# Optimization experiments

Measured on AMD Instinct MI355X. Metric: run time of the kernel, lower is better.

## Reference

```python
import jax, jax.numpy as jnp
import numpy as np

N = 50000   # nodes
E = 800000  # edges
D = 128     # feature / hidden dim
G = 64      # graphs in batch
L = 3       # GCN layers
EPS = 1e-5  # LayerNorm eps (torch default)


def setup_inputs() -> dict:
    key = jax.random.key(0)
    ks = jax.random.split(key, 6)
    x = jax.random.normal(ks[0], (N, D), dtype=jnp.float32)
    edge_index = jax.random.randint(ks[1], (2, E), 0, N)
    batch = jnp.sort(jax.random.randint(ks[2], (N,), 0, G))
    Ws = jax.random.normal(ks[3], (L, D, D), dtype=jnp.float32) / np.sqrt(D).astype(np.float32)
    bs = jnp.zeros((L, D), dtype=jnp.float32)
    gammas = jnp.ones((L, D), dtype=jnp.float32)
    betas = jnp.zeros((L, D), dtype=jnp.float32)
    return {"x": x, "edge_index": edge_index, "batch": batch,
            "Ws": Ws, "bs": bs, "gammas": gammas, "betas": betas,
            "num_graphs": G}


def _layernorm(h, g, b):
    mu = jnp.mean(h, axis=-1, keepdims=True)
    var = jnp.mean((h - mu) ** 2, axis=-1, keepdims=True)
    return g * (h - mu) * jax.lax.rsqrt(var + EPS) + b


def reference(x, edge_index, batch, Ws, bs, gammas, betas, num_graphs):
    n = x.shape[0]
    loop = jnp.arange(n)
    # GCNConv adds self-loops; symmetric normalization on augmented graph
    src = jnp.concatenate([edge_index[0], loop])
    dst = jnp.concatenate([edge_index[1], loop])
    deg = jax.ops.segment_sum(jnp.ones_like(dst, dtype=x.dtype), dst, num_segments=n)
    dinv = jax.lax.rsqrt(jnp.maximum(deg, 1.0))  # deg >= 1 via self-loops
    norm_e = dinv[src] * dinv[dst]               # [E+N]

    h = x
    for i in range(Ws.shape[0]):
        hw = h @ Ws[i]                           # [N, D] dense GEMM
        msg = hw[src] * norm_e[:, None]          # gather + edge scale
        h = jax.ops.segment_sum(msg, dst, num_segments=n) + bs[i]  # scatter-add
        h = jax.nn.relu(_layernorm(h, gammas[i], betas[i]))
        # dropout is identity in eval mode

    # global mean pool over graph ids
    s = jax.ops.segment_sum(h, batch, num_segments=num_graphs)
    cnt = jax.ops.segment_sum(jnp.ones((n,), x.dtype), batch, num_segments=num_graphs)
    return s / jnp.maximum(cnt, 1.0)[:, None]
```

## Files before the change

kernel.cpp:

```cpp
#include <hip/hip_runtime.h>
#include <math.h>


#define NDIM 128
#define LN_EPS 1e-5f
#define NGRAPH 64
#define EPB 2048
#define CSR_CAP 8192

typedef __attribute__((ext_vector_type(8))) short short8;
typedef __attribute__((ext_vector_type(8))) ushort ushort8;
typedef __attribute__((ext_vector_type(4))) float f32x4;

__device__ __forceinline__ ushort f2bf(float f) {
    unsigned u = __float_as_uint(f);
    return (ushort)((u + 0x7FFF + ((u >> 16) & 1)) >> 16);
}
__device__ __forceinline__ float bf2f(ushort b) {
    return __uint_as_float(((unsigned)b) << 16);
}

__device__ __forceinline__ uint block_excl_scan(uint v, uint* s) {
    int t = threadIdx.x;
    s[t] = v; __syncthreads();
    #pragma unroll
    for (int off = 1; off < 256; off <<= 1) {
        uint x = (t >= off) ? s[t - off] : 0u;
        __syncthreads();
        s[t] += x;
        __syncthreads();
    }
    uint incl = s[t];
    __syncthreads();
    return incl - v;
}


__global__ __launch_bounds__(256) void k_build1(const int* __restrict__ src, const int* __restrict__ dst,
                                                uint* __restrict__ hist, uint* __restrict__ arena, int E) {
    __shared__ uint h[256], s[256], rank[256];
    int t = threadIdx.x, b = blockIdx.x;
    h[t] = 0; __syncthreads();
    int e0 = b * EPB;
    #pragma unroll
    for (int i = 0; i < 8; i++) {
        int e = e0 + i * 256 + t;
        if (e < E) atomicAdd(&h[((uint)dst[e]) >> 8], 1u);
    }
    __syncthreads();
    uint cnt = h[t];
    uint off = block_excl_scan(cnt, s);
    hist[(size_t)b * 257 + t] = off;
    if (t == 0) hist[(size_t)b * 257 + 256] = (uint)(min(E - e0, EPB));
    rank[t] = off;
    __syncthreads();
    #pragma unroll
    for (int i = 0; i < 8; i++) {
        int e = e0 + i * 256 + t;
        if (e < E) {
            uint d = (uint)dst[e], sv = (uint)src[e];
            uint bin = d >> 8;
            uint r = atomicAdd(&rank[bin], 1u);
            arena[(size_t)b * EPB + r] = (d << 16) | sv;
        }
    }
}


__global__ __launch_bounds__(256) void k_sort2b(const uint* __restrict__ arena, const uint* __restrict__ hist,
                                                const int* __restrict__ batch,
                                                ushort* __restrict__ csr, int2* __restrict__ bd,
                                                float* __restrict__ dinv,
                                                int* __restrict__ gstart, int* __restrict__ gend,
                                                const float* __restrict__ Ws, ushort* __restrict__ Wt,
                                                int N, int NB, int EB) {
    __shared__ uint h[256], nbase[256], s[256];
    __shared__ uint coff[512], csz[512];
    int t = threadIdx.x, b = blockIdx.x;
    if (b >= NB) {
        int l = b - NB;
        const float* wsrc = Ws + (size_t)l * NDIM * NDIM;
        char* o = (char*)(Wt + (size_t)l * NDIM * NDIM);
        for (int idx = t; idx < NDIM * NDIM; idx += 256) {
            int k = idx >> 7, nn = idx & 127;
            int byte = ((nn * NDIM + k) * 2) ^ ((nn & 7) << 4);
            *(ushort*)(o + byte) = f2bf(wsrc[idx]);
        }
        return;
    }
    for (int r = t; r < EB; r += 256) {
        uint o  = hist[(size_t)r * 257 + b];
        uint nx = (b < 255) ? hist[(size_t)r * 257 + b + 1] : hist[(size_t)r * 257 + 256];
        coff[r] = r * EPB + o;
        csz[r]  = nx - o;
    }
    h[t] = 0; __syncthreads();
    for (int r = t; r < EB; r += 256) {
        uint c0 = coff[r], cn = csz[r];
        for (uint j = 0; j < cn; j++)
            atomicAdd(&h[(arena[c0 + j] >> 16) & 255u], 1u);
    }
    __syncthreads();
    uint dg = h[t];
    uint excl = block_excl_scan((dg + 3u) & ~3u, s);
    uint myb = (uint)b * CSR_CAP + excl;
    nbase[t] = myb;
    int n = b * 256 + t;
    if (n < N) {
        bd[n] = make_int2((int)myb, (int)dg);
        dinv[n] = rsqrtf((float)(dg + 1u));
        int g = batch[n];
        if (n == 0 || batch[n - 1] != g) gstart[g] = n;
        if (n == N - 1 || batch[n + 1] != g) gend[g] = n + 1;
    }
    h[t] = 0; __syncthreads();
    for (int r = t; r < EB; r += 256) {
        uint c0 = coff[r], cn = csz[r];
        for (uint j = 0; j < cn; j++) {
            uint e = arena[c0 + j];
            uint bin = (e >> 16) & 255u;
            uint rk = atomicAdd(&h[bin], 1u);
            csr[nbase[bin] + rk] = (ushort)(e & 0xFFFFu);
        }
    }
}


template <bool AF32>
__global__ __launch_bounds__(256) void k_gemm(const void* __restrict__ Ap, const ushort* __restrict__ Wt,
                                              ushort* __restrict__ C, const float* __restrict__ dinv, int N) {
    __shared__ char sW[32768];
    __shared__ ushort sC[64 * NDIM];
    int tid = threadIdx.x;
    {
        const float4* g = (const float4*)Wt;
        float4* s = (float4*)sW;
        #pragma unroll
        for (int i = 0; i < 8; i++) s[tid + 256 * i] = g[tid + 256 * i];
    }
    __syncthreads();

    int wave = tid >> 6, lane = tid & 63;
    int l15 = lane & 15, lhi = lane >> 4;
    int rw = blockIdx.x * 64 + wave * 16;

    f32x4 acc[8];
    #pragma unroll
    for (int n = 0; n < 8; n++) acc[n] = f32x4{0.f, 0.f, 0.f, 0.f};

    const float*  Af = (const float*)Ap;
    const ushort* Ab = (const ushort*)Ap;

    #pragma unroll
    for (int ks = 0; ks < 4; ks++) {
        int k = ks * 32 + lhi * 8;
        short8 a = short8{};
        int r = rw + l15;
        if (r < N) {
            if (AF32) {
                float4 v0 = *(const float4*)&Af[(size_t)r * NDIM + k];
                float4 v1 = *(const float4*)&Af[(size_t)r * NDIM + k + 4];
                short8 t;
                t[0] = (short)f2bf(v0.x); t[1] = (short)f2bf(v0.y);
                t[2] = (short)f2bf(v0.z); t[3] = (short)f2bf(v0.w);
                t[4] = (short)f2bf(v1.x); t[5] = (short)f2bf(v1.y);
                t[6] = (short)f2bf(v1.z); t[7] = (short)f2bf(v1.w);
                a = t;
            } else {
                a = *(const short8*)&Ab[(size_t)r * NDIM + k];
            }
        }
        #pragma unroll
        for (int n = 0; n < 8; n++) {
            int nn = n * 16 + l15;
            int byte = (nn * 256 + k * 2) ^ ((nn & 7) << 4);
            short8 b = *(const short8*)(sW + byte);
            acc[n] = __builtin_amdgcn_mfma_f32_16x16x32_bf16(a, b, acc[n], 0, 0, 0);
        }
    }

    #pragma unroll
    for (int r = 0; r < 4; r++) {
        int row = rw + lhi * 4 + r;
        float dn = (row < N) ? dinv[row] : 0.f;
        #pragma unroll
        for (int n = 0; n < 8; n++)
            sC[(wave * 16 + lhi * 4 + r) * NDIM + n * 16 + l15] = f2bf(acc[n][r] * dn);
    }
    __syncthreads();
    int row0 = blockIdx.x * 64;
    #pragma unroll
    for (int i = 0; i < 4; i++) {
        int flat = tid + i * 256;
        int row = flat >> 4, c8 = (flat & 15) * 8;
        int gr = row0 + row;
        if (gr < N)
            *(short8*)&C[(size_t)gr * NDIM + c8] = *(const short8*)&sC[row * NDIM + c8];
    }
}


__global__ __launch_bounds__(256) void k_agg(const ushort* __restrict__ hw, ushort* __restrict__ out,
                                             const float* __restrict__ dinv, const int2* __restrict__ bd,
                                             const ushort* __restrict__ csr,
                                             const float* __restrict__ bias, const float* __restrict__ gamma,
                                             const float* __restrict__ beta, int N) {
    int gtid = blockIdx.x * 256 + threadIdx.x;
    int n = gtid >> 5;
    int l4 = threadIdx.x & 31;
    if (n >= N) return;

    const ushort4* hv = (const ushort4*)hw;
    ushort4 sv = hv[(size_t)n * 32 + l4];
    float a0 = bf2f(sv.x), a1 = bf2f(sv.y), a2 = bf2f(sv.z), a3 = bf2f(sv.w);

    int2 bdv = bd[n];
    int b0 = bdv.x, dg = bdv.y;
    int nfull = dg & ~7;
    ushort4 sa, sb;
    if (nfull > 0) {
        sa = *(const ushort4*)&csr[b0];
        sb = *(const ushort4*)&csr[b0 + 4];
    }
    for (int i = 0; i < nfull; i += 8) {
        ushort4 ca = sa, cb = sb;
        if (i + 8 < nfull) {
            sa = *(const ushort4*)&csr[b0 + i + 8];
            sb = *(const ushort4*)&csr[b0 + i + 12];
        }
        ushort4 t0 = hv[(size_t)ca.x * 32 + l4];
        ushort4 t1 = hv[(size_t)ca.y * 32 + l4];
        ushort4 t2 = hv[(size_t)ca.z * 32 + l4];
        ushort4 t3 = hv[(size_t)ca.w * 32 + l4];
        ushort4 t4 = hv[(size_t)cb.x * 32 + l4];
        ushort4 t5 = hv[(size_t)cb.y * 32 + l4];
        ushort4 t6 = hv[(size_t)cb.z * 32 + l4];
        ushort4 t7 = hv[(size_t)cb.w * 32 + l4];
        a0 += bf2f(t0.x) + bf2f(t1.x) + bf2f(t2.x) + bf2f(t3.x)
            + bf2f(t4.x) + bf2f(t5.x) + bf2f(t6.x) + bf2f(t7.x);
        a1 += bf2f(t0.y) + bf2f(t1.y) + bf2f(t2.y) + bf2f(t3.y)
            + bf2f(t4.y) + bf2f(t5.y) + bf2f(t6.y) + bf2f(t7.y);
        a2 += bf2f(t0.z) + bf2f(t1.z) + bf2f(t2.z) + bf2f(t3.z)
            + bf2f(t4.z) + bf2f(t5.z) + bf2f(t6.z) + bf2f(t7.z);
        a3 += bf2f(t0.w) + bf2f(t1.w) + bf2f(t2.w) + bf2f(t3.w)
            + bf2f(t4.w) + bf2f(t5.w) + bf2f(t6.w) + bf2f(t7.w);
    }
    for (int i = nfull; i < dg; i++) {
        int s = csr[b0 + i];
        ushort4 t = hv[(size_t)s * 32 + l4];
        a0 += bf2f(t.x); a1 += bf2f(t.y); a2 += bf2f(t.z); a3 += bf2f(t.w);
    }

    float dn = dinv[n];
    a0 *= dn; a1 *= dn; a2 *= dn; a3 *= dn;

    float4 bv = ((const float4*)bias)[l4];
    a0 += bv.x; a1 += bv.y; a2 += bv.z; a3 += bv.w;

    float s1 = a0 + a1 + a2 + a3;
    float s2 = a0 * a0 + a1 * a1 + a2 * a2 + a3 * a3;
    #pragma unroll
    for (int o = 1; o < 32; o <<= 1) {
        s1 += __shfl_xor(s1, o);
        s2 += __shfl_xor(s2, o);
    }
    float mu = s1 * (1.f / NDIM);
    float var = s2 * (1.f / NDIM) - mu * mu;
    float rs = rsqrtf(var + LN_EPS);

    float4 gv = ((const float4*)gamma)[l4];
    float4 be = ((const float4*)beta)[l4];
    ushort4 y;
    y.x = f2bf(fmaxf(gv.x * (a0 - mu) * rs + be.x, 0.f));
    y.y = f2bf(fmaxf(gv.y * (a1 - mu) * rs + be.y, 0.f));
    y.z = f2bf(fmaxf(gv.z * (a2 - mu) * rs + be.z, 0.f));
    y.w = f2bf(fmaxf(gv.w * (a3 - mu) * rs + be.w, 0.f));
    ((ushort4*)out)[(size_t)n * 32 + l4] = y;
}


__global__ __launch_bounds__(256) void k_pool2(const ushort* __restrict__ h, const int* __restrict__ gstart,
                                               const int* __restrict__ gend, float* __restrict__ out) {
    __shared__ float ps[16][128];
    int t = threadIdx.x, g = blockIdx.x;
    int st = gstart[g], en = gend[g];
    int rslot = t >> 4, dc = (t & 15) * 8;
    float acc[8] = {0.f, 0.f, 0.f, 0.f, 0.f, 0.f, 0.f, 0.f};
    for (int r = st + rslot; r < en; r += 16) {
        ushort8 v = *(const ushort8*)&h[(size_t)r * NDIM + dc];
        #pragma unroll
        for (int j = 0; j < 8; j++) acc[j] += bf2f(v[j]);
    }
    #pragma unroll
    for (int j = 0; j < 8; j++) ps[rslot][dc + j] = acc[j];
    __syncthreads();
    if (t < 128) {
        float s = 0.f;
        #pragma unroll
        for (int k = 0; k < 16; k++) s += ps[k][t];
        float c = (float)(en - st);
        out[g * NDIM + t] = s / fmaxf(c, 1.f);
    }
}


extern "C" void kernel_launch(void* const* d_in, const int* in_sizes, int n_in,
                              void* d_out, int out_size, void* d_ws, size_t ws_size,
                              hipStream_t stream) {
    const float* x      = (const float*)d_in[0];
    const int*   ei     = (const int*)d_in[1];
    const int*   batch  = (const int*)d_in[2];
    const float* Ws     = (const float*)d_in[3];
    const float* bs     = (const float*)d_in[4];
    const float* gammas = (const float*)d_in[5];
    const float* betas  = (const float*)d_in[6];
    float* out = (float*)d_out;

    int N = in_sizes[0] / NDIM;
    int E = in_sizes[1] / 2;
    const int* src = ei;
    const int* dst = ei + E;
    int EB = (E + EPB - 1) / EPB;
    int NB = (N + 255) / 256;

    char* w = (char*)d_ws;
    auto alloc = [&](size_t bytes) { char* p = w; w += (bytes + 255) & ~(size_t)255; return p; };
    uint*   hist   = (uint*)alloc((size_t)EB * 257 * 4);
    uint*   arena  = (uint*)alloc((size_t)EB * EPB * 4);
    ushort* csr    = (ushort*)alloc((size_t)NB * CSR_CAP * 2);
    int2*   bd     = (int2*)alloc((size_t)N * 8);
    float*  dinv   = (float*)alloc((size_t)N * 4);
    int*    gse    = (int*)alloc(2 * NGRAPH * 4);
    int*    gstart = gse;
    int*    gend   = gse + NGRAPH;
    ushort* Wt     = (ushort*)alloc((size_t)3 * NDIM * NDIM * 2);
    ushort* bufA   = (ushort*)alloc((size_t)N * NDIM * 2);
    ushort* bufB   = (ushort*)alloc((size_t)N * NDIM * 2);

    k_build1<<<EB, 256, 0, stream>>>(src, dst, hist, arena, E);
    k_sort2b<<<NB + 3, 256, 0, stream>>>(arena, hist, batch, csr, bd, dinv,
                                         gstart, gend, Ws, Wt, N, NB, EB);

    int gGemm = (N + 63) / 64;
    int gAgg  = (N * 32 + 255) / 256;
    for (int l = 0; l < 3; l++) {
        const ushort* wl = Wt + (size_t)l * NDIM * NDIM;
        if (l == 0)
            k_gemm<true><<<gGemm, 256, 0, stream>>>((const void*)x, wl, bufB, dinv, N);
        else
            k_gemm<false><<<gGemm, 256, 0, stream>>>((const void*)bufA, wl, bufB, dinv, N);
        k_agg<<<gAgg, 256, 0, stream>>>(bufB, bufA, dinv, bd, csr,
                                        bs + l * NDIM, gammas + l * NDIM, betas + l * NDIM, N);
    }

    k_pool2<<<NGRAPH, 256, 0, stream>>>(bufA, gstart, gend, out);
}
```

Before: 272.4 us.

## Fuse aggregation+LayerNorm of layer i with GEMM of layer i+1

```diff
diff --git a/kernel.cpp b/kernel.cpp
--- a/kernel.cpp
+++ b/kernel.cpp
@@ -126,9 +126,8 @@
 }
 
 
-template <bool AF32>
-__global__ __launch_bounds__(256) void k_gemm(const void* __restrict__ Ap, const ushort* __restrict__ Wt,
-                                              ushort* __restrict__ C, const float* __restrict__ dinv, int N) {
+__global__ __launch_bounds__(256) void k_gemm0(const float* __restrict__ Af, const ushort* __restrict__ Wt,
+                                               ushort* __restrict__ C, const float* __restrict__ dinv, int N) {
     __shared__ char sW[32768];
     __shared__ ushort sC[64 * NDIM];
     int tid = threadIdx.x;
@@ -148,27 +147,20 @@
     #pragma unroll
     for (int n = 0; n < 8; n++) acc[n] = f32x4{0.f, 0.f, 0.f, 0.f};
 
-    const float*  Af = (const float*)Ap;
-    const ushort* Ab = (const ushort*)Ap;
-
     #pragma unroll
     for (int ks = 0; ks < 4; ks++) {
         int k = ks * 32 + lhi * 8;
         short8 a = short8{};
         int r = rw + l15;
         if (r < N) {
-            if (AF32) {
-                float4 v0 = *(const float4*)&Af[(size_t)r * NDIM + k];
-                float4 v1 = *(const float4*)&Af[(size_t)r * NDIM + k + 4];
-                short8 t;
-                t[0] = (short)f2bf(v0.x); t[1] = (short)f2bf(v0.y);
-                t[2] = (short)f2bf(v0.z); t[3] = (short)f2bf(v0.w);
-                t[4] = (short)f2bf(v1.x); t[5] = (short)f2bf(v1.y);
-                t[6] = (short)f2bf(v1.z); t[7] = (short)f2bf(v1.w);
-                a = t;
-            } else {
-                a = *(const short8*)&Ab[(size_t)r * NDIM + k];
-            }
+            float4 v0 = *(const float4*)&Af[(size_t)r * NDIM + k];
+            float4 v1 = *(const float4*)&Af[(size_t)r * NDIM + k + 4];
+            short8 t;
+            t[0] = (short)f2bf(v0.x); t[1] = (short)f2bf(v0.y);
+            t[2] = (short)f2bf(v0.z); t[3] = (short)f2bf(v0.w);
+            t[4] = (short)f2bf(v1.x); t[5] = (short)f2bf(v1.y);
+            t[6] = (short)f2bf(v1.z); t[7] = (short)f2bf(v1.w);
+            a = t;
         }
         #pragma unroll
         for (int n = 0; n < 8; n++) {
@@ -200,82 +192,138 @@
 }
 
 
-__global__ __launch_bounds__(256) void k_agg(const ushort* __restrict__ hw, ushort* __restrict__ out,
-                                             const float* __restrict__ dinv, const int2* __restrict__ bd,
-                                             const ushort* __restrict__ csr,
-                                             const float* __restrict__ bias, const float* __restrict__ gamma,
-                                             const float* __restrict__ beta, int N) {
-    int gtid = blockIdx.x * 256 + threadIdx.x;
-    int n = gtid >> 5;
-    int l4 = threadIdx.x & 31;
-    if (n >= N) return;
-
-    const ushort4* hv = (const ushort4*)hw;
-    ushort4 sv = hv[(size_t)n * 32 + l4];
-    float a0 = bf2f(sv.x), a1 = bf2f(sv.y), a2 = bf2f(sv.z), a3 = bf2f(sv.w);
-
-    int2 bdv = bd[n];
-    int b0 = bdv.x, dg = bdv.y;
-    int nfull = dg & ~7;
-    ushort4 sa, sb;
-    if (nfull > 0) {
-        sa = *(const ushort4*)&csr[b0];
-        sb = *(const ushort4*)&csr[b0 + 4];
-    }
-    for (int i = 0; i < nfull; i += 8) {
-        ushort4 ca = sa, cb = sb;
-        if (i + 8 < nfull) {
-            sa = *(const ushort4*)&csr[b0 + i + 8];
-            sb = *(const ushort4*)&csr[b0 + i + 12];
-        }
-        ushort4 t0 = hv[(size_t)ca.x * 32 + l4];
-        ushort4 t1 = hv[(size_t)ca.y * 32 + l4];
-        ushort4 t2 = hv[(size_t)ca.z * 32 + l4];
-        ushort4 t3 = hv[(size_t)ca.w * 32 + l4];
-        ushort4 t4 = hv[(size_t)cb.x * 32 + l4];
-        ushort4 t5 = hv[(size_t)cb.y * 32 + l4];
-        ushort4 t6 = hv[(size_t)cb.z * 32 + l4];
-        ushort4 t7 = hv[(size_t)cb.w * 32 + l4];
-        a0 += bf2f(t0.x) + bf2f(t1.x) + bf2f(t2.x) + bf2f(t3.x)
-            + bf2f(t4.x) + bf2f(t5.x) + bf2f(t6.x) + bf2f(t7.x);
-        a1 += bf2f(t0.y) + bf2f(t1.y) + bf2f(t2.y) + bf2f(t3.y)
-            + bf2f(t4.y) + bf2f(t5.y) + bf2f(t6.y) + bf2f(t7.y);
-        a2 += bf2f(t0.z) + bf2f(t1.z) + bf2f(t2.z) + bf2f(t3.z)
-            + bf2f(t4.z) + bf2f(t5.z) + bf2f(t6.z) + bf2f(t7.z);
-        a3 += bf2f(t0.w) + bf2f(t1.w) + bf2f(t2.w) + bf2f(t3.w)
-            + bf2f(t4.w) + bf2f(t5.w) + bf2f(t6.w) + bf2f(t7.w);
-    }
-    for (int i = nfull; i < dg; i++) {
-        int s = csr[b0 + i];
-        ushort4 t = hv[(size_t)s * 32 + l4];
-        a0 += bf2f(t.x); a1 += bf2f(t.y); a2 += bf2f(t.z); a3 += bf2f(t.w);
-    }
-
-    float dn = dinv[n];
-    a0 *= dn; a1 *= dn; a2 *= dn; a3 *= dn;
-
-    float4 bv = ((const float4*)bias)[l4];
-    a0 += bv.x; a1 += bv.y; a2 += bv.z; a3 += bv.w;
-
-    float s1 = a0 + a1 + a2 + a3;
-    float s2 = a0 * a0 + a1 * a1 + a2 * a2 + a3 * a3;
-    #pragma unroll
-    for (int o = 1; o < 32; o <<= 1) {
-        s1 += __shfl_xor(s1, o);
-        s2 += __shfl_xor(s2, o);
-    }
-    float mu = s1 * (1.f / NDIM);
-    float var = s2 * (1.f / NDIM) - mu * mu;
-    float rs = rsqrtf(var + LN_EPS);
-
-    float4 gv = ((const float4*)gamma)[l4];
-    float4 be = ((const float4*)beta)[l4];
-    ushort4 y;
-    y.x = f2bf(fmaxf(gv.x * (a0 - mu) * rs + be.x, 0.f));
-    y.y = f2bf(fmaxf(gv.y * (a1 - mu) * rs + be.y, 0.f));
-    y.z = f2bf(fmaxf(gv.z * (a2 - mu) * rs + be.z, 0.f));
-    y.w = f2bf(fmaxf(gv.w * (a3 - mu) * rs + be.w, 0.f));
-    ((ushort4*)out)[(size_t)n * 32 + l4] = y;
+template <bool GEMM>
+__global__ __launch_bounds__(256) void k_fused(const ushort* __restrict__ hw_in, ushort* __restrict__ outbuf,
+                                               const float* __restrict__ dinv, const int2* __restrict__ bd,
+                                               const ushort* __restrict__ csr,
+                                               const float* __restrict__ bias, const float* __restrict__ gamma,
+                                               const float* __restrict__ beta,
+                                               const ushort* __restrict__ Wt, int N) {
+    __shared__ char sW[32768];
+    __shared__ ushort sA[64 * NDIM];
+    int tid = threadIdx.x;
+    if (GEMM) {
+        const float4* g = (const float4*)Wt;
+        float4* s = (float4*)sW;
+        #pragma unroll
+        for (int i = 0; i < 8; i++) s[tid + 256 * i] = g[tid + 256 * i];
+    }
+
+    int nb = blockIdx.x * 64;
+    int hwid = tid >> 5, l4 = tid & 31;
+    const ushort4* hv = (const ushort4*)hw_in;
+    const float4 bv = ((const float4*)bias)[l4];
+    const float4 gv = ((const float4*)gamma)[l4];
+    const float4 be = ((const float4*)beta)[l4];
+
+    for (int i = 0; i < 8; i++) {
+        int n = nb + hwid * 8 + i;
+        ushort4 y = make_ushort4(0, 0, 0, 0);
+        if (n < N) {
+            ushort4 sv = hv[(size_t)n * 32 + l4];
+            float a0 = bf2f(sv.x), a1 = bf2f(sv.y), a2 = bf2f(sv.z), a3 = bf2f(sv.w);
+            int2 bdv = bd[n];
+            int b0 = bdv.x, dg = bdv.y;
+            int nfull = dg & ~7;
+            ushort4 sa, sb;
+            if (nfull > 0) {
+                sa = *(const ushort4*)&csr[b0];
+                sb = *(const ushort4*)&csr[b0 + 4];
+            }
+            for (int j = 0; j < nfull; j += 8) {
+                ushort4 ca = sa, cb = sb;
+                if (j + 8 < nfull) {
+                    sa = *(const ushort4*)&csr[b0 + j + 8];
+                    sb = *(const ushort4*)&csr[b0 + j + 12];
+                }
+                ushort4 t0 = hv[(size_t)ca.x * 32 + l4];
+                ushort4 t1 = hv[(size_t)ca.y * 32 + l4];
+                ushort4 t2 = hv[(size_t)ca.z * 32 + l4];
+                ushort4 t3 = hv[(size_t)ca.w * 32 + l4];
+                ushort4 t4 = hv[(size_t)cb.x * 32 + l4];
+                ushort4 t5 = hv[(size_t)cb.y * 32 + l4];
+                ushort4 t6 = hv[(size_t)cb.z * 32 + l4];
+                ushort4 t7 = hv[(size_t)cb.w * 32 + l4];
+                a0 += bf2f(t0.x) + bf2f(t1.x) + bf2f(t2.x) + bf2f(t3.x)
+                    + bf2f(t4.x) + bf2f(t5.x) + bf2f(t6.x) + bf2f(t7.x);
+                a1 += bf2f(t0.y) + bf2f(t1.y) + bf2f(t2.y) + bf2f(t3.y)
+                    + bf2f(t4.y) + bf2f(t5.y) + bf2f(t6.y) + bf2f(t7.y);
+                a2 += bf2f(t0.z) + bf2f(t1.z) + bf2f(t2.z) + bf2f(t3.z)
+                    + bf2f(t4.z) + bf2f(t5.z) + bf2f(t6.z) + bf2f(t7.z);
+                a3 += bf2f(t0.w) + bf2f(t1.w) + bf2f(t2.w) + bf2f(t3.w)
+                    + bf2f(t4.w) + bf2f(t5.w) + bf2f(t6.w) + bf2f(t7.w);
+            }
+            for (int j = nfull; j < dg; j++) {
+                int s = csr[b0 + j];
+                ushort4 t = hv[(size_t)s * 32 + l4];
+                a0 += bf2f(t.x); a1 += bf2f(t.y); a2 += bf2f(t.z); a3 += bf2f(t.w);
+            }
+            float dn = dinv[n];
+            a0 = a0 * dn + bv.x; a1 = a1 * dn + bv.y;
+            a2 = a2 * dn + bv.z; a3 = a3 * dn + bv.w;
+            float s1 = a0 + a1 + a2 + a3;
+            float s2 = a0 * a0 + a1 * a1 + a2 * a2 + a3 * a3;
+            #pragma unroll
+            for (int o = 1; o < 32; o <<= 1) {
+                s1 += __shfl_xor(s1, o);
+                s2 += __shfl_xor(s2, o);
+            }
+            float mu = s1 * (1.f / NDIM);
+            float var = s2 * (1.f / NDIM) - mu * mu;
+            float rs = rsqrtf(var + LN_EPS);
+            y.x = f2bf(fmaxf(gv.x * (a0 - mu) * rs + be.x, 0.f));
+            y.y = f2bf(fmaxf(gv.y * (a1 - mu) * rs + be.y, 0.f));
+            y.z = f2bf(fmaxf(gv.z * (a2 - mu) * rs + be.z, 0.f));
+            y.w = f2bf(fmaxf(gv.w * (a3 - mu) * rs + be.w, 0.f));
+        }
+        if (GEMM) {
+            int row = hwid * 8 + i;
+            int byte = (row * 256 + 8 * l4) ^ ((row & 7) << 4);
+            *(ushort4*)((char*)sA + byte) = y;
+        } else if (n < N) {
+            ((ushort4*)outbuf)[(size_t)n * 32 + l4] = y;
+        }
+    }
+    if (!GEMM) return;
+    __syncthreads();
+
+    int wave = tid >> 6, lane = tid & 63;
+    int l15 = lane & 15, lhi = lane >> 4;
+    f32x4 acc[8];
+    #pragma unroll
+    for (int n = 0; n < 8; n++) acc[n] = f32x4{0.f, 0.f, 0.f, 0.f};
+    #pragma unroll
+    for (int ks = 0; ks < 4; ks++) {
+        int k = ks * 32 + lhi * 8;
+        int rloc = wave * 16 + l15;
+        short8 a = *(const short8*)((char*)sA + ((rloc * 256 + k * 2) ^ ((rloc & 7) << 4)));
+        #pragma unroll
+        for (int n = 0; n < 8; n++) {
+            int nn = n * 16 + l15;
+            int byte = (nn * 256 + k * 2) ^ ((nn & 7) << 4);
+            short8 b = *(const short8*)(sW + byte);
+            acc[n] = __builtin_amdgcn_mfma_f32_16x16x32_bf16(a, b, acc[n], 0, 0, 0);
+        }
+    }
+    __syncthreads();
+    #pragma unroll
+    for (int r = 0; r < 4; r++) {
+        int rloc = wave * 16 + lhi * 4 + r;
+        int row = nb + rloc;
+        float dn = (row < N) ? dinv[row] : 0.f;
+        #pragma unroll
+        for (int n = 0; n < 8; n++)
+            sA[rloc * NDIM + n * 16 + l15] = f2bf(acc[n][r] * dn);
+    }
+    __syncthreads();
+    #pragma unroll
+    for (int i = 0; i < 4; i++) {
+        int flat = tid + i * 256;
+        int row = flat >> 4, c8 = (flat & 15) * 8;
+        int gr = nb + row;
+        if (gr < N)
+            *(short8*)&outbuf[(size_t)gr * NDIM + c8] = *(const short8*)&sA[row * NDIM + c8];
+    }
 }
 
 
@@ -341,17 +389,16 @@
     k_sort2b<<<NB + 3, 256, 0, stream>>>(arena, hist, batch, csr, bd, dinv,
                                          gstart, gend, Ws, Wt, N, NB, EB);
 
-    int gGemm = (N + 63) / 64;
-    int gAgg  = (N * 32 + 255) / 256;
-    for (int l = 0; l < 3; l++) {
-        const ushort* wl = Wt + (size_t)l * NDIM * NDIM;
-        if (l == 0)
-            k_gemm<true><<<gGemm, 256, 0, stream>>>((const void*)x, wl, bufB, dinv, N);
-        else
-            k_gemm<false><<<gGemm, 256, 0, stream>>>((const void*)bufA, wl, bufB, dinv, N);
-        k_agg<<<gAgg, 256, 0, stream>>>(bufB, bufA, dinv, bd, csr,
-                                        bs + l * NDIM, gammas + l * NDIM, betas + l * NDIM, N);
-    }
+    int gRow = (N + 63) / 64;
+    k_gemm0<<<gRow, 256, 0, stream>>>(x, Wt, bufB, dinv, N);
+    k_fused<true><<<gRow, 256, 0, stream>>>(bufB, bufA, dinv, bd, csr,
+                                            bs, gammas, betas, Wt + (size_t)NDIM * NDIM, N);
+    k_fused<true><<<gRow, 256, 0, stream>>>(bufA, bufB, dinv, bd, csr,
+                                            bs + NDIM, gammas + NDIM, betas + NDIM,
+                                            Wt + (size_t)2 * NDIM * NDIM, N);
+    k_fused<false><<<gRow, 256, 0, stream>>>(bufB, bufA, dinv, bd, csr,
+                                             bs + 2 * NDIM, gammas + 2 * NDIM, betas + 2 * NDIM,
+                                             (const ushort*)nullptr, N);
 
     k_pool2<<<NGRAPH, 256, 0, stream>>>(bufA, gstart, gend, out);
 }
```

New measurement: 364.2 us. 1.34x slower.
